# Kernel optimization log

Measured on AMD Instinct MI355X. Metric: run time of the kernel, lower is better.

## Reference

```python
import jax, jax.numpy as jnp
import numpy as np

N = 10000       # nodes
E = 320000      # random edges (self-loops added separately)
IN_SIZE = 2
UNITS = 64
B = 32


def setup_inputs() -> dict:
    # --- build normalized Laplacian edges (matches calculate_laplacian) ---
    rng = np.random.default_rng(0)
    rows = np.concatenate([rng.integers(0, N, E), np.arange(N)]).astype(np.int32)
    cols = np.concatenate([rng.integers(0, N, E), np.arange(N)]).astype(np.int32)
    vals = np.ones(E + N, dtype=np.float32)  # A + I entries
    rowsum = np.zeros(N, dtype=np.float64)
    np.add.at(rowsum, rows, vals.astype(np.float64))
    d = np.where(rowsum > 0, rowsum ** -0.5, 0.0).astype(np.float32)
    # normalized_adj: M = D^-1/2 A^T D^-1/2  ->  M[c, r] = d[r]*d[c]*A[r, c]
    m_rows = jnp.asarray(cols, dtype=jnp.int32)
    m_cols = jnp.asarray(rows, dtype=jnp.int32)
    m_vals = jnp.asarray(vals * d[rows] * d[cols])

    key = jax.random.key(0)
    k = jax.random.split(key, 6)
    F = UNITS + IN_SIZE
    stdv1 = 1.0 / np.sqrt(2 * UNITS)
    stdv2 = 1.0 / np.sqrt(UNITS)
    w1 = jax.random.uniform(k[0], (F, 2 * UNITS), jnp.float32, -stdv1, stdv1)
    b1 = jax.random.uniform(k[1], (2 * UNITS,), jnp.float32, -stdv1, stdv1)
    w2 = jax.random.uniform(k[2], (F, UNITS), jnp.float32, -stdv2, stdv2)
    b2 = jax.random.uniform(k[3], (UNITS,), jnp.float32, -stdv2, stdv2)
    inputs = jax.random.normal(k[4], (B, N * IN_SIZE), jnp.float32)
    state = jax.random.normal(k[5], (B, N * UNITS), jnp.float32)
    return {"inputs": inputs, "state": state, "m_rows": m_rows, "m_cols": m_cols,
            "m_vals": m_vals, "w1": w1, "b1": b1, "w2": w2, "b2": b2}


def _gc(inputs, state, m_rows, m_cols, m_vals, w, b, out_size):
    # [B, N, F] with F = in_size + units
    x_s = jnp.concatenate(
        [inputs.reshape(B, N, IN_SIZE), state.reshape(B, N, UNITS)], axis=2)
    f = x_s.shape[2]
    x0 = jnp.transpose(x_s, (1, 2, 0)).reshape(N, f * B)  # einsum ijk->jki, flatten
    # sparse spmm: x1 = M @ x0
    x1 = jax.ops.segment_sum(m_vals[:, None] * x0[m_cols], m_rows, num_segments=N)
    x = jnp.transpose(x1.reshape(N, f, B), (2, 0, 1)).reshape(B * N, f)  # ijk->kij
    x = x @ w + b
    return x.reshape(B, N * out_size)


def reference(inputs, state, m_rows, m_cols, m_vals, w1, b1, w2, b2):
    value = jax.nn.sigmoid(_gc(inputs, state, m_rows, m_cols, m_vals, w1, b1, 2 * UNITS))
    # NOTE: faithful to original: split of FLATTENED [B, N*2U] at the midpoint
    r, u = jnp.split(value, 2, axis=1)
    c = jax.nn.relu(_gc(inputs, r * state, m_rows, m_cols, m_vals, w2, b2, UNITS))
    new_h = u * state + (1.0 - u) * c
    return new_h
```

## Files before the change

kernel.cpp:

```cpp
#include <hip/hip_runtime.h>
#include <hip/hip_fp16.h>
#include <cstdint>
#include <cstdio>

#define N_NODES 10000
#define BATCH   32
#define UNITS   64
#define F_DIM   66
#define XROW    2048
#define KPAD    96
#define ASTR    104
#define GRP     8

typedef float v2f __attribute__((ext_vector_type(2)));
typedef float f32x4 __attribute__((ext_vector_type(4)));
typedef _Float16 half8 __attribute__((ext_vector_type(8)));

__device__ __forceinline__ float sigmoidf(float x) {
  return 1.0f / (1.0f + __expf(-x));
}

__global__ __launch_bounds__(256) void hist_k(const int* __restrict__ rows,
                                              int* __restrict__ counts, int E2,
                                              const float* __restrict__ w1,
                                              const float* __restrict__ w2,
                                              _Float16* __restrict__ w1T,
                                              _Float16* __restrict__ w2T) {
  int e = blockIdx.x * 256 + threadIdx.x;
  if (e < E2) atomicAdd(&counts[rows[e]], 1);
  if (e < 128 * KPAD) {
    int j = e / KPAD, f = e % KPAD;
    w1T[e] = (f < 66) ? (_Float16)w1[f * 128 + j] : (_Float16)0.0f;
  } else if (e < 128 * KPAD + 64 * KPAD) {
    int k = e - 128 * KPAD;
    int j = k / KPAD, f = k % KPAD;
    w2T[k] = (f < 66) ? (_Float16)w2[f * 64 + j] : (_Float16)0.0f;
  }
}

__global__ __launch_bounds__(256) void scan_k(const int* __restrict__ counts,
                                              int* __restrict__ rowptr,
                                              int* __restrict__ wofs, int n) {
  __shared__ int lbuf[10240];
  __shared__ int sums[256];
  int t = threadIdx.x;
  for (int i = t; i < N_NODES / 4; i += 256)
    reinterpret_cast<int4*>(lbuf)[i] = reinterpret_cast<const int4*>(counts)[i];
  for (int i = N_NODES + t; i < 10240; i += 256) lbuf[i] = 0;
  __syncthreads();
  int base = t * 40;
  int v[40];
  int run = 0;
#pragma unroll
  for (int i = 0; i < 40; ++i) { v[i] = run; run += lbuf[base + i]; }
  sums[t] = run;
  __syncthreads();
  for (int off = 1; off < 256; off <<= 1) {
    int x = (t >= off) ? sums[t - off] : 0;
    __syncthreads();
    sums[t] += x;
    __syncthreads();
  }
  int tbase = (t == 0) ? 0 : sums[t - 1];
#pragma unroll
  for (int i = 0; i < 40; ++i) lbuf[base + i] = tbase + v[i];
  __syncthreads();
  for (int i = t; i < N_NODES / 4; i += 256) {
    int4 w = reinterpret_cast<int4*>(lbuf)[i];
    reinterpret_cast<int4*>(rowptr)[i] = w;
    reinterpret_cast<int4*>(wofs)[i] = w;
  }
  if (t == 255) rowptr[N_NODES] = sums[255];
}

__device__ __forceinline__ void pack_row_fp8(const float* T, int n, int t,
                                             unsigned char* xcat8) {
  int k0 = t * 8;
  int f8 = k0 >> 5;
  int b0 = k0 & 31;
  const float* Ts = &T[(f8 + 2) * 33 + b0];
  int d0 = __builtin_amdgcn_cvt_pk_fp8_f32(Ts[0], Ts[1], 0, false);
  d0     = __builtin_amdgcn_cvt_pk_fp8_f32(Ts[2], Ts[3], d0, true);
  int d1 = __builtin_amdgcn_cvt_pk_fp8_f32(Ts[4], Ts[5], 0, false);
  d1     = __builtin_amdgcn_cvt_pk_fp8_f32(Ts[6], Ts[7], d1, true);
  *reinterpret_cast<uint2*>(xcat8 + (size_t)n * XROW + k0) = make_uint2(d0, d1);
}

__global__ __launch_bounds__(256) void scat_build(const int* __restrict__ rows,
                                                  const int* __restrict__ cols,
                                                  const float* __restrict__ vals,
                                                  int* __restrict__ wofs,
                                                  int2* __restrict__ ecv, int E2,
                                                  const float* __restrict__ inputs,
                                                  const float* __restrict__ state,
                                                  unsigned char* __restrict__ xcat8,
                                                  __half2* __restrict__ xin) {
  int blk = blockIdx.x, t = threadIdx.x;
  if (blk >= N_NODES) {
    int e = (blk - N_NODES) * 256 + t;
    if (e < E2) {
      int r = rows[e];
      int p = atomicAdd(&wofs[r], 1);
      ecv[p] = make_int2(cols[e] << 11, __float_as_int(vals[e]));
    }
    return;
  }
  int n = blk;
  __shared__ float T[66 * 33];
  int f = t & 63, bq = t >> 6;
#pragma unroll
  for (int bb = 0; bb < 8; ++bb) {
    int b = bq + bb * 4;
    T[(f + 2) * 33 + b] = state[(size_t)b * 640000 + (size_t)n * 64 + f];
  }
  if (t < 64) {
    int b0 = t & 31, f0 = t >> 5;
    T[f0 * 33 + b0] = inputs[(size_t)b0 * 20000 + (size_t)n * 2 + f0];
  }
  __syncthreads();
  pack_row_fp8(T, n, t, xcat8);
  if (t < 32) {
    int f0 = t >> 4, b = (t & 15) * 2;
    xin[(size_t)n * 32 + t] = __floats2half2_rn(T[f0 * 33 + b], T[f0 * 33 + b + 1]);
  }
}

__global__ __launch_bounds__(256) void yin_k(const int* __restrict__ rowptr,
                                             const int2* __restrict__ ecv,
                                             const __half* __restrict__ xin,
                                             float* __restrict__ yin) {
  int n = (blockIdx.x * 256 + threadIdx.x) >> 6;
  if (n >= N_NODES) return;
  int lane  = threadIdx.x & 63;
  int eslot = lane >> 4;
  int sub   = lane & 15;
  unsigned sb = (unsigned)sub * 8u;

  float acc0 = 0.0f, acc1 = 0.0f, acc2 = 0.0f, acc3 = 0.0f;
  int s = rowptr[n], e = rowptr[n + 1];
  const char* xb = reinterpret_cast<const char*>(xin);
  for (int ee = s + eslot; ee < e; ee += 4) {
    int2 cv = ecv[ee];
    float v = __int_as_float(cv.y);
    unsigned off = ((unsigned)cv.x >> 4) + sb;
    uint2 raw = *reinterpret_cast<const uint2*>(xb + off);
    __half2 h0 = *reinterpret_cast<__half2*>(&raw.x);
    __half2 h1 = *reinterpret_cast<__half2*>(&raw.y);
    float2 x0 = __half22float2(h0);
    float2 x1 = __half22float2(h1);
    acc0 += v * x0.x; acc1 += v * x0.y;
    acc2 += v * x1.x; acc3 += v * x1.y;
  }
#pragma unroll
  for (int m = 16; m <= 32; m <<= 1) {
    acc0 += __shfl_xor(acc0, m);
    acc1 += __shfl_xor(acc1, m);
    acc2 += __shfl_xor(acc2, m);
    acc3 += __shfl_xor(acc3, m);
  }
  if (eslot == 0) {
    *reinterpret_cast<float4*>(yin + (size_t)n * 64 + sub * 4) =
        make_float4(acc0, acc1, acc2, acc3);
  }
}

__device__ __forceinline__ void consume8f8(uint2 u, float v, v2f* acc) {
  v2f p0 = __builtin_amdgcn_cvt_pk_f32_fp8((int)u.x, false);
  v2f p1 = __builtin_amdgcn_cvt_pk_f32_fp8((int)u.x, true);
  v2f p2 = __builtin_amdgcn_cvt_pk_f32_fp8((int)u.y, false);
  v2f p3 = __builtin_amdgcn_cvt_pk_f32_fp8((int)u.y, true);
  v2f vv = {v, v};
  acc[0] += vv * p0;
  acc[1] += vv * p1;
  acc[2] += vv * p2;
  acc[3] += vv * p3;
}

__device__ __forceinline__ void ld_grp(const int2* __restrict__ ep, int gsz,
                                       const unsigned char* __restrict__ xcat8,
                                       unsigned t8, uint2* r, float* v) {
#pragma unroll
  for (int q = 0; q < GRP; ++q) {
    int2 c = ep[q];
    if (q >= gsz) { c.x = 0; c.y = 0; }
    unsigned off = (unsigned)c.x + t8;
    r[q] = *reinterpret_cast<const uint2*>(xcat8 + off);
    v[q] = __int_as_float(c.y);
  }
}

__device__ __forceinline__ void cons_grp(const uint2* r, const float* v, v2f* acc) {
#pragma unroll
  for (int q = 0; q < GRP; ++q) consume8f8(r[q], v[q], acc);
}

__device__ __forceinline__ void spmm_body(int n, int t,
                                          const int* __restrict__ rowptr,
                                          const int2* __restrict__ ecv,
                                          const unsigned char* __restrict__ xcat8,
                                          const float* __restrict__ yin,
                                          _Float16* accH) {
  v2f acc[4];
#pragma unroll
  for (int i = 0; i < 4; ++i) acc[i] = (v2f){0.0f, 0.0f};

  unsigned t8 = (unsigned)t * 8u;
  int s = rowptr[n], e = rowptr[n + 1];
  int ne = e - s;
  int ng = (ne + GRP - 1) / GRP;
  const int2* ep = ecv + s;

  uint2 rA[GRP], rB[GRP];
  float vA[GRP], vB[GRP];
  ld_grp(ep, ne, xcat8, t8, rA, vA);
  int g = 1;
  for (; g + 1 < ng; g += 2) {
    ld_grp(ep + GRP * g, ne - GRP * g, xcat8, t8, rB, vB);
    cons_grp(rA, vA, acc);
    ld_grp(ep + GRP * (g + 1), ne - GRP * (g + 1), xcat8, t8, rA, vA);
    cons_grp(rB, vB, acc);
  }
  if (g < ng) {
    ld_grp(ep + GRP * g, ne - GRP * g, xcat8, t8, rB, vB);
    cons_grp(rA, vA, acc);
    cons_grp(rB, vB, acc);
  } else {
    cons_grp(rA, vA, acc);
  }

  {
    int f8 = t >> 2;
    int b0 = (t & 3) * 8;
    float a[8] = {acc[0].x, acc[0].y, acc[1].x, acc[1].y,
                  acc[2].x, acc[2].y, acc[3].x, acc[3].y};
    _Float16* dst = accH + (f8 + 2);
#pragma unroll
    for (int i = 0; i < 8; ++i) {
      dst[(b0 + i) * ASTR] = (_Float16)a[i];
    }
  }
  if (t < 64) {
    int f = t >> 5, b = t & 31;
    accH[b * ASTR + f] = (_Float16)yin[(size_t)n * 64 + t];
  }
  for (int id = t; id < 32 * 19; id += 256) {
    int b = id / 19, c = id % 19;
    *reinterpret_cast<unsigned int*>(
        reinterpret_cast<char*>(accH) + b * (ASTR * 2) + 132 + c * 4) = 0u;
  }
  __syncthreads();
}

__global__ __launch_bounds__(256) void gcn1(const int* __restrict__ rowptr,
                                            const int2* __restrict__ ecv,
                                            const unsigned char* __restrict__ xcat8,
                                            const float* __restrict__ yin,
                                            const _Float16* __restrict__ w1T,
                                            const float* __restrict__ b1,
                                            const float* __restrict__ state,
                                            unsigned char* __restrict__ xcat2,
                                            __half* __restrict__ valu) {
  int n = blockIdx.x, t = threadIdx.x;
  __shared__ __align__(16) char smem[32 * 136 * 2];
  _Float16* accH = reinterpret_cast<_Float16*>(smem);

  spmm_body(n, t, rowptr, ecv, xcat8, yin, accH);

  int wv = t >> 6, l = t & 63;
  int mt = wv & 1, ntb = (wv >> 1) * 4;
  int lr = l & 15, lg = l >> 4;
  const _Float16* aB = accH + (size_t)(mt * 16 + lr) * ASTR + lg * 8;
  half8 afr0 = *reinterpret_cast<const half8*>(aB);
  half8 afr1 = *reinterpret_cast<const half8*>(aB + 32);
  half8 afr2 = *reinterpret_cast<const half8*>(aB + 64);
  __syncthreads();
  _Float16* vstage = reinterpret_cast<_Float16*>(smem);

#pragma unroll
  for (int tt = 0; tt < 4; ++tt) {
    int j = (ntb + tt) * 16 + lr;
    const _Float16* wB = w1T + (size_t)j * KPAD + lg * 8;
    f32x4 c = {0.0f, 0.0f, 0.0f, 0.0f};
    c = __builtin_amdgcn_mfma_f32_16x16x32_f16(afr0, *reinterpret_cast<const half8*>(wB), c, 0, 0, 0);
    c = __builtin_amdgcn_mfma_f32_16x16x32_f16(afr1, *reinterpret_cast<const half8*>(wB + 32), c, 0, 0, 0);
    c = __builtin_amdgcn_mfma_f32_16x16x32_f16(afr2, *reinterpret_cast<const half8*>(wB + 64), c, 0, 0, 0);
    float bj = b1[j];
#pragma unroll
    for (int i = 0; i < 4; ++i) {
      int b = mt * 16 + lg * 4 + i;
      vstage[b * 136 + j] = (_Float16)sigmoidf(c[i] + bj);
    }
  }
  __syncthreads();

  if (n < 5000) {
    int nn_i = t >> 7;
    int f    = t & 63;
    int bg   = (t >> 6) & 1;
    int nn = n * 2 + nn_i;
    int jj = nn_i * 64 + f;
    const float* sp = state + (size_t)nn * 64 + f;
    const _Float16* vp = vstage + jj;
    int bbase = bg * 16;
    unsigned int d[4];
#pragma unroll
    for (int q = 0; q < 4; ++q) {
      int b0 = bbase + q * 4;
      float x0 = (float)vp[(b0 + 0) * 136] * sp[(size_t)(b0 + 0) * 640000];
      float x1 = (float)vp[(b0 + 1) * 136] * sp[(size_t)(b0 + 1) * 640000];
      float x2 = (float)vp[(b0 + 2) * 136] * sp[(size_t)(b0 + 2) * 640000];
      float x3 = (float)vp[(b0 + 3) * 136] * sp[(size_t)(b0 + 3) * 640000];
      int dd = __builtin_amdgcn_cvt_pk_fp8_f32(x0, x1, 0, false);
      dd     = __builtin_amdgcn_cvt_pk_fp8_f32(x2, x3, dd, true);
      d[q] = (unsigned)dd;
    }
    *reinterpret_cast<uint4*>(xcat2 + (size_t)nn * XROW + f * 32 + bbase) =
        make_uint4(d[0], d[1], d[2], d[3]);
  } else {
    int b = t >> 3, jg = t & 7;
    const uint4* src = reinterpret_cast<const uint4*>(vstage + b * 136 + jg * 16);
    uint4 q0 = src[0];
    uint4 q1 = src[1];
    __half* vb = valu + (size_t)(n - 5000) * 4096 + b * 128 + jg * 16;
    *reinterpret_cast<uint4*>(vb) = q0;
    *reinterpret_cast<uint4*>(vb + 8) = q1;
  }
}

__global__ __launch_bounds__(256) void gcn2(const int* __restrict__ rowptr,
                                            const int2* __restrict__ ecv,
                                            const unsigned char* __restrict__ xcat2,
                                            const float* __restrict__ yin,
                                            const _Float16* __restrict__ w2T,
                                            const float* __restrict__ b2,
                                            const __half* __restrict__ valu,
                                            const float* __restrict__ state,
                                            float* __restrict__ out) {
  int n = blockIdx.x, t = threadIdx.x;
  __shared__ __align__(16) char smem[32 * 68 * 4];
  _Float16* accH = reinterpret_cast<_Float16*>(smem);

  spmm_body(n, t, rowptr, ecv, xcat2, yin, accH);

  int wv = t >> 6, l = t & 63;
  int mt = wv & 1, ntb = (wv >> 1) * 2;
  int lr = l & 15, lg = l >> 4;
  const _Float16* aB = accH + (size_t)(mt * 16 + lr) * ASTR + lg * 8;
  half8 afr0 = *reinterpret_cast<const half8*>(aB);
  half8 afr1 = *reinterpret_cast<const half8*>(aB + 32);
  half8 afr2 = *reinterpret_cast<const half8*>(aB + 64);
  __syncthreads();
  float* ostage = reinterpret_cast<float*>(smem);

#pragma unroll
  for (int tt = 0; tt < 2; ++tt) {
    int j = (ntb + tt) * 16 + lr;
    const _Float16* wB = w2T + (size_t)j * KPAD + lg * 8;
    f32x4 c = {0.0f, 0.0f, 0.0f, 0.0f};
    c = __builtin_amdgcn_mfma_f32_16x16x32_f16(afr0, *reinterpret_cast<const half8*>(wB), c, 0, 0, 0);
    c = __builtin_amdgcn_mfma_f32_16x16x32_f16(afr1, *reinterpret_cast<const half8*>(wB + 32), c, 0, 0, 0);
    c = __builtin_amdgcn_mfma_f32_16x16x32_f16(afr2, *reinterpret_cast<const half8*>(wB + 64), c, 0, 0, 0);
    float bj = b2[j];
#pragma unroll
    for (int i = 0; i < 4; ++i) {
      int b = mt * 16 + lg * 4 + i;
      ostage[b * 68 + j] = fmaxf(c[i] + bj, 0.0f);
    }
  }
  __syncthreads();

  int bg = t >> 4, jg = t & 15;
  int n2 = n >> 1, no = n & 1;
  const __half* up = valu + (size_t)n2 * 4096 + (size_t)no * 64 + jg * 4;
#pragma unroll
  for (int i = 0; i < 2; ++i) {
    int b = bg * 2 + i;
    size_t idx = (size_t)b * 640000 + (size_t)n * 64 + jg * 4;
    float4 sv = *reinterpret_cast<const float4*>(state + idx);
    float4 cc = *reinterpret_cast<const float4*>(ostage + b * 68 + jg * 4);
    union { uint2 u; __half2 h[2]; } pk;
    pk.u = *reinterpret_cast<const uint2*>(up + (size_t)b * 128);
    float2 u01 = __half22float2(pk.h[0]);
    float2 u23 = __half22float2(pk.h[1]);
    float4 h;
    h.x = u01.x * sv.x + (1.0f - u01.x) * cc.x;
    h.y = u01.y * sv.y + (1.0f - u01.y) * cc.y;
    h.z = u23.x * sv.z + (1.0f - u23.x) * cc.z;
    h.w = u23.y * sv.w + (1.0f - u23.y) * cc.w;
    *reinterpret_cast<float4*>(out + idx) = h;
  }
}

static inline size_t alignup(size_t x) { return (x + 255) & ~(size_t)255; }

extern "C" void kernel_launch(void* const* d_in, const int* in_sizes, int n_in,
                              void* d_out, int out_size, void* d_ws, size_t ws_size,
                              hipStream_t stream) {
  const float* inputs = (const float*)d_in[0];
  const float* state  = (const float*)d_in[1];
  const int*   m_rows = (const int*)d_in[2];
  const int*   m_cols = (const int*)d_in[3];
  const float* m_vals = (const float*)d_in[4];
  const float* w1     = (const float*)d_in[5];
  const float* b1     = (const float*)d_in[6];
  const float* w2     = (const float*)d_in[7];
  const float* b2     = (const float*)d_in[8];
  float* out = (float*)d_out;

  const int N  = N_NODES;
  const int E2 = in_sizes[2];

  char* ws = (char*)d_ws;
  size_t off = 0;
  int* counts = (int*)(ws + off); off = alignup(off + (size_t)N * 4);
  int* rowptr = (int*)(ws + off); off = alignup(off + (size_t)(N + 1) * 4);
  int* wofs   = (int*)(ws + off); off = alignup(off + (size_t)N * 4);
  int2* ecv   = (int2*)(ws + off); off = alignup(off + (size_t)E2 * 8 + 256);
  unsigned char* xcat8 = (unsigned char*)(ws + off); off = alignup(off + (size_t)N * XROW);
  unsigned char* xcat2 = (unsigned char*)(ws + off); off = alignup(off + (size_t)N * XROW);
  __half* valu = (__half*)(ws + off); off = alignup(off + (size_t)5000 * 4096 * 2);
  float* yin  = (float*)(ws + off); off = alignup(off + (size_t)N * 64 * 4);
  __half* xin = (__half*)(ws + off); off = alignup(off + (size_t)N * 64 * 2);
  _Float16* w1T = (_Float16*)(ws + off); off = alignup(off + (size_t)128 * KPAD * 2);
  _Float16* w2T = (_Float16*)(ws + off); off = alignup(off + (size_t)64 * KPAD * 2);
  if (off > ws_size) { return; }

  hipMemsetAsync(counts, 0, (size_t)N * 4, stream);

  int eb = (E2 + 255) / 256;
  hipLaunchKernelGGL(hist_k,     dim3(eb), dim3(256), 0, stream, m_rows, counts, E2,
                     w1, w2, w1T, w2T);
  hipLaunchKernelGGL(scan_k,     dim3(1),  dim3(256), 0, stream, counts, rowptr, wofs, N);
  hipLaunchKernelGGL(scat_build, dim3(N + eb), dim3(256), 0, stream,
                     m_rows, m_cols, m_vals, wofs, ecv, E2,
                     inputs, state, xcat8, (__half2*)xin);
  hipLaunchKernelGGL(yin_k,      dim3((N + 3) / 4), dim3(256), 0, stream,
                     rowptr, ecv, xin, yin);
  hipLaunchKernelGGL(gcn1,       dim3(N),  dim3(256), 0, stream, rowptr, ecv,
                     xcat8, yin, w1T, b1, state, xcat2, valu);
  hipLaunchKernelGGL(gcn2,       dim3(N),  dim3(256), 0, stream, rowptr, ecv,
                     xcat2, yin, w2T, b2, valu, state, out);
}
```

Before: 424.6 us.

## Split gather feature matrix into batch slices so each block handles four nodes

The fp8 feature matrix moves from one 2048-byte row per node to eight batch slices of 256 bytes per node. Each block now handles four nodes, one per wave, for a four-batch slice, and the grid grows from 10000 to 20000 blocks. Each slice is 2.5 MB, so the random-column gathers should hit a working set small enough to stay in cache, and each lane loads 4 bytes per edge. The cost is that edge lists and rowptr are read eight times instead of once, and the MFMA tiles now cover only 16 rows per block.

```diff
diff --git a/kernel.cpp b/kernel.cpp
--- a/kernel.cpp
+++ b/kernel.cpp
@@ -6,11 +6,11 @@
 #define N_NODES 10000
 #define BATCH   32
 #define UNITS   64
-#define F_DIM   66
-#define XROW    2048
 #define KPAD    96
 #define ASTR    104
 #define GRP     8
+#define NGRP    2500
+#define NBLK    20000
 
 typedef float v2f __attribute__((ext_vector_type(2)));
 typedef float f32x4 __attribute__((ext_vector_type(4)));
@@ -73,19 +73,6 @@
   if (t == 255) rowptr[N_NODES] = sums[255];
 }
 
-__device__ __forceinline__ void pack_row_fp8(const float* T, int n, int t,
-                                             unsigned char* xcat8) {
-  int k0 = t * 8;
-  int f8 = k0 >> 5;
-  int b0 = k0 & 31;
-  const float* Ts = &T[(f8 + 2) * 33 + b0];
-  int d0 = __builtin_amdgcn_cvt_pk_fp8_f32(Ts[0], Ts[1], 0, false);
-  d0     = __builtin_amdgcn_cvt_pk_fp8_f32(Ts[2], Ts[3], d0, true);
-  int d1 = __builtin_amdgcn_cvt_pk_fp8_f32(Ts[4], Ts[5], 0, false);
-  d1     = __builtin_amdgcn_cvt_pk_fp8_f32(Ts[6], Ts[7], d1, true);
-  *reinterpret_cast<uint2*>(xcat8 + (size_t)n * XROW + k0) = make_uint2(d0, d1);
-}
-
 __global__ __launch_bounds__(256) void scat_build(const int* __restrict__ rows,
                                                   const int* __restrict__ cols,
                                                   const float* __restrict__ vals,
@@ -93,35 +80,33 @@
                                                   int2* __restrict__ ecv, int E2,
                                                   const float* __restrict__ inputs,
                                                   const float* __restrict__ state,
-                                                  unsigned char* __restrict__ xcat8,
-                                                  __half2* __restrict__ xin) {
+                                                  unsigned char* __restrict__ xcat,
+                                                  __half* __restrict__ xin) {
   int blk = blockIdx.x, t = threadIdx.x;
-  if (blk >= N_NODES) {
-    int e = (blk - N_NODES) * 256 + t;
+  if (blk >= NBLK) {
+    int e = (blk - NBLK) * 256 + t;
     if (e < E2) {
       int r = rows[e];
       int p = atomicAdd(&wofs[r], 1);
-      ecv[p] = make_int2(cols[e] << 11, __float_as_int(vals[e]));
+      ecv[p] = make_int2(cols[e] << 8, __float_as_int(vals[e]));
     }
     return;
   }
-  int n = blk;
-  __shared__ float T[66 * 33];
-  int f = t & 63, bq = t >> 6;
-#pragma unroll
-  for (int bb = 0; bb < 8; ++bb) {
-    int b = bq + bb * 4;
-    T[(f + 2) * 33 + b] = state[(size_t)b * 640000 + (size_t)n * 64 + f];
-  }
-  if (t < 64) {
-    int b0 = t & 31, f0 = t >> 5;
-    T[f0 * 33 + b0] = inputs[(size_t)b0 * 20000 + (size_t)n * 2 + f0];
-  }
-  __syncthreads();
-  pack_row_fp8(T, n, t, xcat8);
-  if (t < 32) {
-    int f0 = t >> 4, b = (t & 15) * 2;
-    xin[(size_t)n * 32 + t] = __floats2half2_rn(T[f0 * 33 + b], T[f0 * 33 + b + 1]);
+  int g = blk >> 3, s = blk & 7;
+  int wv = t >> 6, lane = t & 63;
+  int n = g * 4 + wv;
+  float x[4];
+#pragma unroll
+  for (int bi = 0; bi < 4; ++bi)
+    x[bi] = state[(size_t)(s * 4 + bi) * 640000 + (size_t)n * 64 + lane];
+  int d = __builtin_amdgcn_cvt_pk_fp8_f32(x[0], x[1], 0, false);
+  d     = __builtin_amdgcn_cvt_pk_fp8_f32(x[2], x[3], d, true);
+  *reinterpret_cast<unsigned*>(xcat + (((size_t)(s * N_NODES + n)) << 8) + lane * 4) =
+      (unsigned)d;
+  if (lane < 8) {
+    int bi = lane >> 1, f = lane & 1;
+    float v = inputs[(size_t)(s * 4 + bi) * 20000 + (size_t)n * 2 + f];
+    xin[(size_t)n * 64 + f * 32 + s * 4 + bi] = (__half)v;
   }
 }
 
@@ -142,7 +127,7 @@
   for (int ee = s + eslot; ee < e; ee += 4) {
     int2 cv = ecv[ee];
     float v = __int_as_float(cv.y);
-    unsigned off = ((unsigned)cv.x >> 4) + sb;
+    unsigned off = ((unsigned)cv.x >> 1) + sb;
     uint2 raw = *reinterpret_cast<const uint2*>(xb + off);
     __half2 h0 = *reinterpret_cast<__half2*>(&raw.x);
     __half2 h1 = *reinterpret_cast<__half2*>(&raw.y);
@@ -164,166 +149,161 @@
   }
 }
 
-__device__ __forceinline__ void consume8f8(uint2 u, float v, v2f* acc) {
-  v2f p0 = __builtin_amdgcn_cvt_pk_f32_fp8((int)u.x, false);
-  v2f p1 = __builtin_amdgcn_cvt_pk_f32_fp8((int)u.x, true);
-  v2f p2 = __builtin_amdgcn_cvt_pk_f32_fp8((int)u.y, false);
-  v2f p3 = __builtin_amdgcn_cvt_pk_f32_fp8((int)u.y, true);
-  v2f vv = {v, v};
-  acc[0] += vv * p0;
-  acc[1] += vv * p1;
-  acc[2] += vv * p2;
-  acc[3] += vv * p3;
-}
-
-__device__ __forceinline__ void ld_grp(const int2* __restrict__ ep, int gsz,
-                                       const unsigned char* __restrict__ xcat8,
-                                       unsigned t8, uint2* r, float* v) {
+__device__ __forceinline__ void ld_grp4(const int2* __restrict__ ep, int gsz,
+                                        const char* __restrict__ xb,
+                                        unsigned* r, float* v) {
 #pragma unroll
   for (int q = 0; q < GRP; ++q) {
     int2 c = ep[q];
     if (q >= gsz) { c.x = 0; c.y = 0; }
-    unsigned off = (unsigned)c.x + t8;
-    r[q] = *reinterpret_cast<const uint2*>(xcat8 + off);
+    r[q] = *reinterpret_cast<const unsigned*>(xb + (unsigned)c.x);
     v[q] = __int_as_float(c.y);
   }
 }
 
-__device__ __forceinline__ void cons_grp(const uint2* r, const float* v, v2f* acc) {
-#pragma unroll
-  for (int q = 0; q < GRP; ++q) consume8f8(r[q], v[q], acc);
-}
-
-__device__ __forceinline__ void spmm_body(int n, int t,
-                                          const int* __restrict__ rowptr,
-                                          const int2* __restrict__ ecv,
-                                          const unsigned char* __restrict__ xcat8,
-                                          const float* __restrict__ yin,
-                                          _Float16* accH) {
-  v2f acc[4];
-#pragma unroll
-  for (int i = 0; i < 4; ++i) acc[i] = (v2f){0.0f, 0.0f};
-
-  unsigned t8 = (unsigned)t * 8u;
-  int s = rowptr[n], e = rowptr[n + 1];
-  int ne = e - s;
+__device__ __forceinline__ void cons_grp4(const unsigned* r, const float* v, v2f* acc) {
+#pragma unroll
+  for (int q = 0; q < GRP; ++q) {
+    v2f p0 = __builtin_amdgcn_cvt_pk_f32_fp8((int)r[q], false);
+    v2f p1 = __builtin_amdgcn_cvt_pk_f32_fp8((int)r[q], true);
+    v2f vv = {v[q], v[q]};
+    acc[0] += vv * p0;
+    acc[1] += vv * p1;
+  }
+}
+
+__device__ __forceinline__ void spmm_slice(int g, int s, int t,
+                                           const int* __restrict__ rowptr,
+                                           const int2* __restrict__ ecv,
+                                           const unsigned char* __restrict__ xcat,
+                                           const float* __restrict__ yin,
+                                           _Float16* accH) {
+  int wv = t >> 6, lane = t & 63;
+  int n = g * 4 + wv;
+  const char* xb = reinterpret_cast<const char*>(xcat) +
+                   (((size_t)(s * N_NODES)) << 8) + (unsigned)lane * 4;
+  int se = __builtin_amdgcn_readfirstlane(rowptr[n]);
+  int ee = __builtin_amdgcn_readfirstlane(rowptr[n + 1]);
+  int ne = ee - se;
   int ng = (ne + GRP - 1) / GRP;
-  const int2* ep = ecv + s;
-
-  uint2 rA[GRP], rB[GRP];
+  const int2* ep = ecv + se;
+
+  v2f acc[2];
+  acc[0] = (v2f){0.0f, 0.0f};
+  acc[1] = (v2f){0.0f, 0.0f};
+
+  unsigned rA[GRP], rB[GRP];
   float vA[GRP], vB[GRP];
-  ld_grp(ep, ne, xcat8, t8, rA, vA);
-  int g = 1;
-  for (; g + 1 < ng; g += 2) {
-    ld_grp(ep + GRP * g, ne - GRP * g, xcat8, t8, rB, vB);
-    cons_grp(rA, vA, acc);
-    ld_grp(ep + GRP * (g + 1), ne - GRP * (g + 1), xcat8, t8, rA, vA);
-    cons_grp(rB, vB, acc);
-  }
-  if (g < ng) {
-    ld_grp(ep + GRP * g, ne - GRP * g, xcat8, t8, rB, vB);
-    cons_grp(rA, vA, acc);
-    cons_grp(rB, vB, acc);
+  ld_grp4(ep, ne, xb, rA, vA);
+  int gg = 1;
+  for (; gg + 1 < ng; gg += 2) {
+    ld_grp4(ep + GRP * gg, ne - GRP * gg, xb, rB, vB);
+    cons_grp4(rA, vA, acc);
+    ld_grp4(ep + GRP * (gg + 1), ne - GRP * (gg + 1), xb, rA, vA);
+    cons_grp4(rB, vB, acc);
+  }
+  if (gg < ng) {
+    ld_grp4(ep + GRP * gg, ne - GRP * gg, xb, rB, vB);
+    cons_grp4(rA, vA, acc);
+    cons_grp4(rB, vB, acc);
   } else {
-    cons_grp(rA, vA, acc);
+    cons_grp4(rA, vA, acc);
   }
 
   {
-    int f8 = t >> 2;
-    int b0 = (t & 3) * 8;
-    float a[8] = {acc[0].x, acc[0].y, acc[1].x, acc[1].y,
-                  acc[2].x, acc[2].y, acc[3].x, acc[3].y};
-    _Float16* dst = accH + (f8 + 2);
-#pragma unroll
-    for (int i = 0; i < 8; ++i) {
-      dst[(b0 + i) * ASTR] = (_Float16)a[i];
-    }
-  }
-  if (t < 64) {
-    int f = t >> 5, b = t & 31;
-    accH[b * ASTR + f] = (_Float16)yin[(size_t)n * 64 + t];
-  }
-  for (int id = t; id < 32 * 19; id += 256) {
-    int b = id / 19, c = id % 19;
-    *reinterpret_cast<unsigned int*>(
-        reinterpret_cast<char*>(accH) + b * (ASTR * 2) + 132 + c * 4) = 0u;
+    _Float16* dst = accH + (size_t)(wv * 4) * ASTR + 2 + lane;
+    dst[0 * ASTR] = (_Float16)acc[0].x;
+    dst[1 * ASTR] = (_Float16)acc[0].y;
+    dst[2 * ASTR] = (_Float16)acc[1].x;
+    dst[3 * ASTR] = (_Float16)acc[1].y;
+  }
+  if (t < 240) {
+    int m = t / 15, d2 = t % 15;
+    *reinterpret_cast<unsigned*>(
+        reinterpret_cast<char*>(accH) + m * (ASTR * 2) + 132 + d2 * 4) = 0u;
+  } else {
+    int m = t - 240;
+    int bi = m & 3, ni = m >> 2;
+    int nn = g * 4 + ni;
+    accH[m * ASTR + 0] = (_Float16)yin[(size_t)nn * 64 + s * 4 + bi];
+    accH[m * ASTR + 1] = (_Float16)yin[(size_t)nn * 64 + 32 + s * 4 + bi];
   }
   __syncthreads();
 }
 
 __global__ __launch_bounds__(256) void gcn1(const int* __restrict__ rowptr,
                                             const int2* __restrict__ ecv,
-                                            const unsigned char* __restrict__ xcat8,
+                                            const unsigned char* __restrict__ xcat,
                                             const float* __restrict__ yin,
                                             const _Float16* __restrict__ w1T,
                                             const float* __restrict__ b1,
                                             const float* __restrict__ state,
                                             unsigned char* __restrict__ xcat2,
                                             __half* __restrict__ valu) {
-  int n = blockIdx.x, t = threadIdx.x;
-  __shared__ __align__(16) char smem[32 * 136 * 2];
+  int blk = blockIdx.x, t = threadIdx.x;
+  int g = blk >> 3, s = blk & 7;
+  __shared__ __align__(16) char smem[16 * 136 * 2];
   _Float16* accH = reinterpret_cast<_Float16*>(smem);
 
-  spmm_body(n, t, rowptr, ecv, xcat8, yin, accH);
-
-  int wv = t >> 6, l = t & 63;
-  int mt = wv & 1, ntb = (wv >> 1) * 4;
-  int lr = l & 15, lg = l >> 4;
-  const _Float16* aB = accH + (size_t)(mt * 16 + lr) * ASTR + lg * 8;
-  half8 afr0 = *reinterpret_cast<const half8*>(aB);
-  half8 afr1 = *reinterpret_cast<const half8*>(aB + 32);
-  half8 afr2 = *reinterpret_cast<const half8*>(aB + 64);
+  spmm_slice(g, s, t, rowptr, ecv, xcat, yin, accH);
+
+  int wv = t >> 6, lane = t & 63;
+  int lr = lane & 15, lg = lane >> 4;
+  const _Float16* aB = accH + (size_t)lr * ASTR + lg * 8;
+  half8 a0 = *reinterpret_cast<const half8*>(aB);
+  half8 a1 = *reinterpret_cast<const half8*>(aB + 32);
+  half8 a2 = *reinterpret_cast<const half8*>(aB + 64);
   __syncthreads();
   _Float16* vstage = reinterpret_cast<_Float16*>(smem);
 
 #pragma unroll
-  for (int tt = 0; tt < 4; ++tt) {
-    int j = (ntb + tt) * 16 + lr;
+  for (int tt = 0; tt < 2; ++tt) {
+    int j = (wv * 2 + tt) * 16 + lr;
     const _Float16* wB = w1T + (size_t)j * KPAD + lg * 8;
     f32x4 c = {0.0f, 0.0f, 0.0f, 0.0f};
-    c = __builtin_amdgcn_mfma_f32_16x16x32_f16(afr0, *reinterpret_cast<const half8*>(wB), c, 0, 0, 0);
-    c = __builtin_amdgcn_mfma_f32_16x16x32_f16(afr1, *reinterpret_cast<const half8*>(wB + 32), c, 0, 0, 0);
-    c = __builtin_amdgcn_mfma_f32_16x16x32_f16(afr2, *reinterpret_cast<const half8*>(wB + 64), c, 0, 0, 0);
+    c = __builtin_amdgcn_mfma_f32_16x16x32_f16(a0, *reinterpret_cast<const half8*>(wB), c, 0, 0, 0);
+    c = __builtin_amdgcn_mfma_f32_16x16x32_f16(a1, *reinterpret_cast<const half8*>(wB + 32), c, 0, 0, 0);
+    c = __builtin_amdgcn_mfma_f32_16x16x32_f16(a2, *reinterpret_cast<const half8*>(wB + 64), c, 0, 0, 0);
     float bj = b1[j];
 #pragma unroll
     for (int i = 0; i < 4; ++i) {
-      int b = mt * 16 + lg * 4 + i;
-      vstage[b * 136 + j] = (_Float16)sigmoidf(c[i] + bj);
+      vstage[(lg * 4 + i) * 136 + j] = (_Float16)sigmoidf(c[i] + bj);
     }
   }
   __syncthreads();
 
-  if (n < 5000) {
-    int nn_i = t >> 7;
-    int f    = t & 63;
-    int bg   = (t >> 6) & 1;
-    int nn = n * 2 + nn_i;
-    int jj = nn_i * 64 + f;
-    const float* sp = state + (size_t)nn * 64 + f;
-    const _Float16* vp = vstage + jj;
-    int bbase = bg * 16;
-    unsigned int d[4];
-#pragma unroll
-    for (int q = 0; q < 4; ++q) {
-      int b0 = bbase + q * 4;
-      float x0 = (float)vp[(b0 + 0) * 136] * sp[(size_t)(b0 + 0) * 640000];
-      float x1 = (float)vp[(b0 + 1) * 136] * sp[(size_t)(b0 + 1) * 640000];
-      float x2 = (float)vp[(b0 + 2) * 136] * sp[(size_t)(b0 + 2) * 640000];
-      float x3 = (float)vp[(b0 + 3) * 136] * sp[(size_t)(b0 + 3) * 640000];
-      int dd = __builtin_amdgcn_cvt_pk_fp8_f32(x0, x1, 0, false);
-      dd     = __builtin_amdgcn_cvt_pk_fp8_f32(x2, x3, dd, true);
-      d[q] = (unsigned)dd;
+  if (g < 1250) {
+    int node_i = t >> 6, rem = t & 63;
+    int nglob = g * 4 + node_i;
+    int nn = 2 * nglob + (rem >> 5);
+    int f0 = (rem * 2) & 63;
+    int mrow = node_i * 4;
+    int j0 = rem * 2;
+    float2 st[4];
+#pragma unroll
+    for (int bi = 0; bi < 4; ++bi)
+      st[bi] = *reinterpret_cast<const float2*>(
+          state + (size_t)(s * 4 + bi) * 640000 + (size_t)nn * 64 + f0);
+    unsigned dq[2];
+#pragma unroll
+    for (int q = 0; q < 2; ++q) {
+      float y0 = (float)vstage[(mrow + 0) * 136 + j0 + q] * (q ? st[0].y : st[0].x);
+      float y1 = (float)vstage[(mrow + 1) * 136 + j0 + q] * (q ? st[1].y : st[1].x);
+      float y2 = (float)vstage[(mrow + 2) * 136 + j0 + q] * (q ? st[2].y : st[2].x);
+      float y3 = (float)vstage[(mrow + 3) * 136 + j0 + q] * (q ? st[3].y : st[3].x);
+      int dd = __builtin_amdgcn_cvt_pk_fp8_f32(y0, y1, 0, false);
+      dd     = __builtin_amdgcn_cvt_pk_fp8_f32(y2, y3, dd, true);
+      dq[q] = (unsigned)dd;
     }
-    *reinterpret_cast<uint4*>(xcat2 + (size_t)nn * XROW + f * 32 + bbase) =
-        make_uint4(d[0], d[1], d[2], d[3]);
+    *reinterpret_cast<uint2*>(xcat2 + (((size_t)(s * N_NODES + nn)) << 8) + f0 * 4) =
+        make_uint2(dq[0], dq[1]);
   } else {
-    int b = t >> 3, jg = t & 7;
-    const uint4* src = reinterpret_cast<const uint4*>(vstage + b * 136 + jg * 16);
-    uint4 q0 = src[0];
-    uint4 q1 = src[1];
-    __half* vb = valu + (size_t)(n - 5000) * 4096 + b * 128 + jg * 16;
-    *reinterpret_cast<uint4*>(vb) = q0;
-    *reinterpret_cast<uint4*>(vb + 8) = q1;
+    int node_i = t >> 6;
+    int bi = (t >> 4) & 3, jq = (t & 15) * 8;
+    int nm = g * 4 + node_i - 5000;
+    uint4 q0 = *reinterpret_cast<const uint4*>(vstage + (node_i * 4 + bi) * 136 + jq);
+    *reinterpret_cast<uint4*>(
+        valu + ((size_t)(s * 5000 + nm) * 4 + bi) * 128 + jq) = q0;
   }
 }
 
@@ -336,59 +316,55 @@
                                             const __half* __restrict__ valu,
                                             const float* __restrict__ state,
                                             float* __restrict__ out) {
-  int n = blockIdx.x, t = threadIdx.x;
-  __shared__ __align__(16) char smem[32 * 68 * 4];
+  int blk = blockIdx.x, t = threadIdx.x;
+  int g = blk >> 3, s = blk & 7;
+  __shared__ __align__(16) char smem[16 * 68 * 4];
   _Float16* accH = reinterpret_cast<_Float16*>(smem);
 
-  spmm_body(n, t, rowptr, ecv, xcat2, yin, accH);
-
-  int wv = t >> 6, l = t & 63;
-  int mt = wv & 1, ntb = (wv >> 1) * 2;
-  int lr = l & 15, lg = l >> 4;
-  const _Float16* aB = accH + (size_t)(mt * 16 + lr) * ASTR + lg * 8;
-  half8 afr0 = *reinterpret_cast<const half8*>(aB);
-  half8 afr1 = *reinterpret_cast<const half8*>(aB + 32);
-  half8 afr2 = *reinterpret_cast<const half8*>(aB + 64);
+  spmm_slice(g, s, t, rowptr, ecv, xcat2, yin, accH);
+
+  int wv = t >> 6, lane = t & 63;
+  int lr = lane & 15, lg = lane >> 4;
+  const _Float16* aB = accH + (size_t)lr * ASTR + lg * 8;
+  half8 a0 = *reinterpret_cast<const half8*>(aB);
+  half8 a1 = *reinterpret_cast<const half8*>(aB + 32);
+  half8 a2 = *reinterpret_cast<const half8*>(aB + 64);
   __syncthreads();
   float* ostage = reinterpret_cast<float*>(smem);
 
-#pragma unroll
-  for (int tt = 0; tt < 2; ++tt) {
-    int j = (ntb + tt) * 16 + lr;
+  {
+    int j = wv * 16 + lr;
     const _Float16* wB = w2T + (size_t)j * KPAD + lg * 8;
     f32x4 c = {0.0f, 0.0f, 0.0f, 0.0f};
-    c = __builtin_amdgcn_mfma_f32_16x16x32_f16(afr0, *reinterpret_cast<const half8*>(wB), c, 0, 0, 0);
-    c = __builtin_amdgcn_mfma_f32_16x16x32_f16(afr1, *reinterpret_cast<const half8*>(wB + 32), c, 0, 0, 0);
-    c = __builtin_amdgcn_mfma_f32_16x16x32_f16(afr2, *reinterpret_cast<const half8*>(wB + 64), c, 0, 0, 0);
+    c = __builtin_amdgcn_mfma_f32_16x16x32_f16(a0, *reinterpret_cast<const half8*>(wB), c, 0, 0, 0);
+    c = __builtin_amdgcn_mfma_f32_16x16x32_f16(a1, *reinterpret_cast<const half8*>(wB + 32), c, 0, 0, 0);
+    c = __builtin_amdgcn_mfma_f32_16x16x32_f16(a2, *reinterpret_cast<const half8*>(wB + 64), c, 0, 0, 0);
     float bj = b2[j];
 #pragma unroll
     for (int i = 0; i < 4; ++i) {
-      int b = mt * 16 + lg * 4 + i;
-      ostage[b * 68 + j] = fmaxf(c[i] + bj, 0.0f);
+      ostage[(lg * 4 + i) * 68 + j] = fmaxf(c[i] + bj, 0.0f);
     }
   }
   __syncthreads();
 
-  int bg = t >> 4, jg = t & 15;
-  int n2 = n >> 1, no = n & 1;
-  const __half* up = valu + (size_t)n2 * 4096 + (size_t)no * 64 + jg * 4;
-#pragma unroll
-  for (int i = 0; i < 2; ++i) {
-    int b = bg * 2 + i;
-    size_t idx = (size_t)b * 640000 + (size_t)n * 64 + jg * 4;
-    float4 sv = *reinterpret_cast<const float4*>(state + idx);
-    float4 cc = *reinterpret_cast<const float4*>(ostage + b * 68 + jg * 4);
-    union { uint2 u; __half2 h[2]; } pk;
-    pk.u = *reinterpret_cast<const uint2*>(up + (size_t)b * 128);
-    float2 u01 = __half22float2(pk.h[0]);
-    float2 u23 = __half22float2(pk.h[1]);
-    float4 h;
-    h.x = u01.x * sv.x + (1.0f - u01.x) * cc.x;
-    h.y = u01.y * sv.y + (1.0f - u01.y) * cc.y;
-    h.z = u23.x * sv.z + (1.0f - u23.x) * cc.z;
-    h.w = u23.y * sv.w + (1.0f - u23.y) * cc.w;
-    *reinterpret_cast<float4*>(out + idx) = h;
-  }
+  int node_i = t >> 6;
+  int bi = (t >> 4) & 3, f0 = (t & 15) * 4;
+  int n = g * 4 + node_i;
+  size_t idx = (size_t)(s * 4 + bi) * 640000 + (size_t)n * 64 + f0;
+  float4 sv = *reinterpret_cast<const float4*>(state + idx);
+  float4 cc = *reinterpret_cast<const float4*>(ostage + (node_i * 4 + bi) * 68 + f0);
+  const __half* up = valu + ((size_t)(s * 5000 + (n >> 1)) * 4 + bi) * 128 +
+                     (n & 1) * 64 + f0;
+  union { uint2 u; __half2 h[2]; } pk;
+  pk.u = *reinterpret_cast<const uint2*>(up);
+  float2 u01 = __half22float2(pk.h[0]);
+  float2 u23 = __half22float2(pk.h[1]);
+  float4 h;
+  h.x = u01.x * sv.x + (1.0f - u01.x) * cc.x;
+  h.y = u01.y * sv.y + (1.0f - u01.y) * cc.y;
+  h.z = u23.x * sv.z + (1.0f - u23.x) * cc.z;
+  h.w = u23.y * sv.w + (1.0f - u23.y) * cc.w;
+  *reinterpret_cast<float4*>(out + idx) = h;
 }
 
 static inline size_t alignup(size_t x) { return (x + 255) & ~(size_t)255; }
@@ -416,8 +392,8 @@
   int* rowptr = (int*)(ws + off); off = alignup(off + (size_t)(N + 1) * 4);
   int* wofs   = (int*)(ws + off); off = alignup(off + (size_t)N * 4);
   int2* ecv   = (int2*)(ws + off); off = alignup(off + (size_t)E2 * 8 + 256);
-  unsigned char* xcat8 = (unsigned char*)(ws + off); off = alignup(off + (size_t)N * XROW);
-  unsigned char* xcat2 = (unsigned char*)(ws + off); off = alignup(off + (size_t)N * XROW);
+  unsigned char* xcat  = (unsigned char*)(ws + off); off = alignup(off + (size_t)8 * N * 256);
+  unsigned char* xcat2 = (unsigned char*)(ws + off); off = alignup(off + (size_t)8 * N * 256);
   __half* valu = (__half*)(ws + off); off = alignup(off + (size_t)5000 * 4096 * 2);
   float* yin  = (float*)(ws + off); off = alignup(off + (size_t)N * 64 * 4);
   __half* xin = (__half*)(ws + off); off = alignup(off + (size_t)N * 64 * 2);
@@ -431,13 +407,13 @@
   hipLaunchKernelGGL(hist_k,     dim3(eb), dim3(256), 0, stream, m_rows, counts, E2,
                      w1, w2, w1T, w2T);
   hipLaunchKernelGGL(scan_k,     dim3(1),  dim3(256), 0, stream, counts, rowptr, wofs, N);
-  hipLaunchKernelGGL(scat_build, dim3(N + eb), dim3(256), 0, stream,
+  hipLaunchKernelGGL(scat_build, dim3(NBLK + eb), dim3(256), 0, stream,
                      m_rows, m_cols, m_vals, wofs, ecv, E2,
-                     inputs, state, xcat8, (__half2*)xin);
+                     inputs, state, xcat, xin);
   hipLaunchKernelGGL(yin_k,      dim3((N + 3) / 4), dim3(256), 0, stream,
                      rowptr, ecv, xin, yin);
-  hipLaunchKernelGGL(gcn1,       dim3(N),  dim3(256), 0, stream, rowptr, ecv,
-                     xcat8, yin, w1T, b1, state, xcat2, valu);
-  hipLaunchKernelGGL(gcn2,       dim3(N),  dim3(256), 0, stream, rowptr, ecv,
+  hipLaunchKernelGGL(gcn1,       dim3(NBLK), dim3(256), 0, stream, rowptr, ecv,
+                     xcat, yin, w1T, b1, state, xcat2, valu);
+  hipLaunchKernelGGL(gcn2,       dim3(NBLK), dim3(256), 0, stream, rowptr, ecv,
                      xcat2, yin, w2T, b2, valu, state, out);
 }
```

Measured after the change: 368.4 us. 13.2% less time.
